# Kernel tuning notes

Hardware: AMD Instinct MI355X
Metric: run time of the kernel (lower is better)

## Reference

```python
import jax, jax.numpy as jnp
import numpy as np

HIDDEN = 512
QK_DIM = HIDDEN // 8  # 64
B, H, W = 32, 32, 32


def conv1x1(x, w, b):
    # 1x1 conv == channel matmul: w [out_c, in_c], x [b, in_c, h, w]
    return jnp.einsum('oc,bchw->bohw', w, x) + b[None, :, None, None]


def setup_inputs() -> dict:
    key = jax.random.key(0)
    ks = jax.random.split(key, 10)
    s = 0.02
    return {
        'x': jax.random.normal(ks[0], (B, HIDDEN, H, W), jnp.float32),
        'pos_embedding': jax.random.normal(ks[1], (1, HIDDEN, 32, 32), jnp.float32),
        'query_w': jax.random.normal(ks[2], (QK_DIM, HIDDEN), jnp.float32) * s,
        'query_b': jax.random.normal(ks[3], (QK_DIM,), jnp.float32) * s,
        'key_w': jax.random.normal(ks[4], (QK_DIM, HIDDEN), jnp.float32) * s,
        'key_b': jax.random.normal(ks[5], (QK_DIM,), jnp.float32) * s,
        'value_w': jax.random.normal(ks[6], (HIDDEN, HIDDEN), jnp.float32) * s,
        'value_b': jax.random.normal(ks[7], (HIDDEN,), jnp.float32) * s,
        'out_w': jax.random.normal(ks[8], (HIDDEN, HIDDEN), jnp.float32) * s,
        'out_b': jax.random.normal(ks[9], (HIDDEN,), jnp.float32) * s,
    }


def reference(x, pos_embedding, query_w, query_b, key_w, key_b,
              value_w, value_b, out_w, out_b):
    b, c, h, w = x.shape
    n = h * w
    x = x + pos_embedding[:, :, :h, :w]
    q = conv1x1(x, query_w, query_b).reshape(b, -1, n)   # [b, d, n]
    k = conv1x1(x, key_w, key_b).reshape(b, -1, n)       # [b, d, n]
    v = conv1x1(x, value_w, value_b).reshape(b, -1, n)   # [b, c, n]
    # scores[b,i,j] = sum_d q[b,d,i] * k[b,d,j]  (no 1/sqrt(d) scaling, faithful)
    scores = jnp.einsum('bdi,bdj->bij', q, k)
    attn = jax.nn.softmax(scores, axis=-1)               # [b, n, n]
    # out[b,c,i] = sum_j v[b,c,j] * attn[b,i,j]
    out = jnp.einsum('bcj,bij->bci', v, attn).reshape(b, c, h, w)
    return conv1x1(out, out_w, out_b)
```

## Files before the change

kernel.cpp:

```cpp
#include <hip/hip_runtime.h>

#define BB 32
#define CC 512
#define DD 64
#define NN 1024
#define GRP 16
#define NGRP (BB / GRP)

typedef float4 f4;
typedef __attribute__((ext_vector_type(8))) short bf16x8;
typedef __attribute__((ext_vector_type(4))) float f32x4;
typedef __attribute__((ext_vector_type(4))) unsigned short us4;
typedef __attribute__((ext_vector_type(8))) unsigned short us8;

__device__ inline unsigned short bf16rn(float f) {
  union { float f; unsigned u; } v; v.f = f;
  unsigned r = v.u + 0x7fff + ((v.u >> 16) & 1);
  return (unsigned short)(r >> 16);
}

__device__ inline void gl_lds16(const void* g, void* l) {
  __builtin_amdgcn_global_load_lds(
      (const __attribute__((address_space(1))) unsigned int*)g,
      (__attribute__((address_space(3))) unsigned int*)l, 16, 0, 0);
}

template <int KDIM>
__device__ inline void gemm_core(const unsigned short* __restrict__ A,
                                 const unsigned short* __restrict__ Bt,
                                 int m0, int n0, int tid,
                                 unsigned short* sA, unsigned short* sB,
                                 f32x4 acc[4][4]) {
  const int wave = tid >> 6, lane = tid & 63;
  const int wm = (wave & 1) * 64, wn = (wave >> 1) * 64;
  const int fm = lane & 15;
  const int kq = lane >> 4;
  const int srow = lane >> 3;
  const int sg   = (lane & 7) ^ srow;

  for (int k0 = 0; k0 < KDIM; k0 += 64) {
#pragma unroll
    for (int t = 0; t < 4; ++t) {
      const int R = wave * 32 + t * 8;
      gl_lds16(A  + (size_t)(m0 + R + srow) * KDIM + k0 + sg * 8, sA + R * 64);
      gl_lds16(Bt + (size_t)(n0 + R + srow) * KDIM + k0 + sg * 8, sB + R * 64);
    }
    __syncthreads();
#pragma unroll
    for (int ks = 0; ks < 2; ++ks) {
      bf16x8 af[4], bfr[4];
#pragma unroll
      for (int i = 0; i < 4; ++i) {
        const int ra = wm + i * 16 + fm;
        const int rb = wn + i * 16 + fm;
        af[i]  = *(const bf16x8*)(sA + ra * 64 + ((ks * 4 + kq) ^ (ra & 7)) * 8);
        bfr[i] = *(const bf16x8*)(sB + rb * 64 + ((ks * 4 + kq) ^ (rb & 7)) * 8);
      }
#pragma unroll
      for (int i = 0; i < 4; ++i)
#pragma unroll
        for (int j = 0; j < 4; ++j)
          acc[i][j] = __builtin_amdgcn_mfma_f32_16x16x32_bf16(af[i], bfr[j], acc[i][j], 0, 0, 0);
    }
    __syncthreads();
  }
}

__global__ __launch_bounds__(256) void prep_w(
    const float* __restrict__ qw, const float* __restrict__ kw, const float* __restrict__ vw,
    const float* __restrict__ qb, const float* __restrict__ kb, const float* __restrict__ vb,
    const float* __restrict__ ow,
    unsigned short* __restrict__ wcat, unsigned short* __restrict__ owb,
    float* __restrict__ bcat) {
  int idx = blockIdx.x * 256 + threadIdx.x;
  if (idx < 640 * 512) {
    int row = idx >> 9;
    float v = (row < 64) ? qw[idx] : (row < 128) ? kw[idx - 64 * 512] : vw[idx - 128 * 512];
    wcat[idx] = bf16rn(v);
    if (idx < 640) bcat[idx] = (idx < 64) ? qb[idx] : (idx < 128) ? kb[idx - 64] : vb[idx - 128];
  } else {
    int j = idx - 640 * 512;
    owb[j] = bf16rn(ow[j]);
  }
}

__global__ __launch_bounds__(256) void prep_x(const float* __restrict__ x,
                                              const float* __restrict__ pos,
                                              unsigned short* __restrict__ A) {
  __shared__ float t[64][65];
  const int b = blockIdx.z, i0 = blockIdx.x * 64, c0 = blockIdx.y * 64;
  const int tid = threadIdx.x;
  const int ci = tid >> 4, il = (tid & 15) * 4;
  const float* xb = x + (size_t)b * CC * NN;
#pragma unroll
  for (int r = 0; r < 4; ++r) {
    int cl = r * 16 + ci;
    f4 xv = *(const f4*)(xb  + (size_t)(c0 + cl) * NN + i0 + il);
    f4 pv = *(const f4*)(pos + (size_t)(c0 + cl) * NN + i0 + il);
    t[cl][il + 0] = xv.x + pv.x;
    t[cl][il + 1] = xv.y + pv.y;
    t[cl][il + 2] = xv.z + pv.z;
    t[cl][il + 3] = xv.w + pv.w;
  }
  __syncthreads();
  const int iw = tid >> 2, cw = (tid & 3) * 16;
  unsigned short* dst = A + ((size_t)b * NN + i0 + iw) * CC + c0 + cw;
  us8 p0, p1;
#pragma unroll
  for (int j = 0; j < 8; ++j) p0[j] = bf16rn(t[cw + j][iw]);
#pragma unroll
  for (int j = 0; j < 8; ++j) p1[j] = bf16rn(t[cw + 8 + j][iw]);
  *(us8*)dst = p0;
  *(us8*)(dst + 8) = p1;
}

__global__ __launch_bounds__(256) void proj_gemm(
    const unsigned short* __restrict__ A, const unsigned short* __restrict__ wcat,
    const float* __restrict__ bcat,
    unsigned short* __restrict__ qo, unsigned short* __restrict__ ko,
    unsigned short* __restrict__ vto) {
  __shared__ unsigned short sA[8192], sB[8192];
  const int b = blockIdx.z, m0 = blockIdx.x * 128, n0 = blockIdx.y * 128;
  const int tid = threadIdx.x, wave = tid >> 6, lane = tid & 63;
  f32x4 acc[4][4];
#pragma unroll
  for (int i = 0; i < 4; ++i)
#pragma unroll
    for (int j = 0; j < 4; ++j) acc[i][j] = (f32x4)(0.0f);

  gemm_core<512>(A + (size_t)b * NN * CC, wcat, m0, n0, tid, sA, sB, acc);

  const int wm = (wave & 1) * 64, wn = (wave >> 1) * 64;
#pragma unroll
  for (int i = 0; i < 4; ++i)
#pragma unroll
    for (int j = 0; j < 4; ++j) {
      int col  = n0 + wn + j * 16 + (lane & 15);
      int rowb = m0 + wm + i * 16 + (lane >> 4) * 4;
      float bias = bcat[col];
      if (col < 64) {
#pragma unroll
        for (int r = 0; r < 4; ++r)
          qo[((size_t)b * NN + rowb + r) * DD + col] = bf16rn(acc[i][j][r] + bias);
      } else if (col < 128) {
#pragma unroll
        for (int r = 0; r < 4; ++r)
          ko[((size_t)b * NN + rowb + r) * DD + col - 64] = bf16rn(acc[i][j][r] + bias);
      } else {
        int c = col - 128;
        us4 pk;
#pragma unroll
        for (int r = 0; r < 4; ++r) pk[r] = bf16rn(acc[i][j][r] + bias);
        *(us4*)(vto + ((size_t)b * CC + c) * NN + rowb) = pk;
      }
    }
}

__global__ __launch_bounds__(256) void stats_kernel(
    const unsigned short* __restrict__ q, const unsigned short* __restrict__ k,
    float2* __restrict__ stats) {
  __shared__ unsigned short sQ[128 * 64];
  __shared__ unsigned short sK[128 * 64];
  __shared__ float2 wred[4][128];

  const int b = blockIdx.y, i0 = blockIdx.x * 128;
  const int tid = threadIdx.x, wave = tid >> 6, lane = tid & 63;
  const int wm = (wave & 1) * 64, wn = (wave >> 1) * 64;
  const int fm = lane & 15, kq = lane >> 4;
  const int srow = lane >> 3, sg = (lane & 7) ^ srow;

  const unsigned short* qb = q + (size_t)b * NN * DD;
  const unsigned short* kb = k + (size_t)b * NN * DD;

#pragma unroll
  for (int t = 0; t < 4; ++t) {
    const int R = wave * 32 + t * 8;
    gl_lds16(qb + (size_t)(i0 + R + srow) * DD + sg * 8, sQ + R * 64);
  }

  bf16x8 aq[4][2];
  float m_l[4][4], l_l[4][4];
#pragma unroll
  for (int i = 0; i < 4; ++i)
#pragma unroll
    for (int r = 0; r < 4; ++r) { m_l[i][r] = -1e30f; l_l[i][r] = 0.f; }

  for (int jt = 0; jt < 8; ++jt) {
    const int j0 = jt * 128;
#pragma unroll
    for (int t = 0; t < 4; ++t) {
      const int R = wave * 32 + t * 8;
      gl_lds16(kb + (size_t)(j0 + R + srow) * DD + sg * 8, sK + R * 64);
    }
    __syncthreads();
    if (jt == 0) {
#pragma unroll
      for (int i = 0; i < 4; ++i)
#pragma unroll
        for (int kd = 0; kd < 2; ++kd) {
          const int ra = wm + i * 16 + fm;
          aq[i][kd] = *(const bf16x8*)(sQ + ra * 64 + ((kd * 4 + kq) ^ (ra & 7)) * 8);
        }
    }
    f32x4 S[4][4];
#pragma unroll
    for (int i = 0; i < 4; ++i)
#pragma unroll
      for (int j = 0; j < 4; ++j) S[i][j] = (f32x4)(0.0f);
#pragma unroll
    for (int kd = 0; kd < 2; ++kd) {
      bf16x8 bk[4];
#pragma unroll
      for (int j = 0; j < 4; ++j) {
        const int rb = wn + j * 16 + fm;
        bk[j] = *(const bf16x8*)(sK + rb * 64 + ((kd * 4 + kq) ^ (rb & 7)) * 8);
      }
#pragma unroll
      for (int i = 0; i < 4; ++i)
#pragma unroll
        for (int j = 0; j < 4; ++j)
          S[i][j] = __builtin_amdgcn_mfma_f32_16x16x32_bf16(aq[i][kd], bk[j], S[i][j], 0, 0, 0);
    }
#pragma unroll
    for (int i = 0; i < 4; ++i)
#pragma unroll
      for (int r = 0; r < 4; ++r) {
        float v0 = S[0 * 0 + i][0][r], v1 = S[i][1][r], v2 = S[i][2][r], v3 = S[i][3][r];
        float mt = fmaxf(fmaxf(v0, v1), fmaxf(v2, v3));
        float lt = __expf(v0 - mt) + __expf(v1 - mt) + __expf(v2 - mt) + __expf(v3 - mt);
        float mo = m_l[i][r];
        float mn = fmaxf(mo, mt);
        l_l[i][r] = l_l[i][r] * __expf(mo - mn) + lt * __expf(mt - mn);
        m_l[i][r] = mn;
      }
    __syncthreads();
  }

#pragma unroll
  for (int i = 0; i < 4; ++i)
#pragma unroll
    for (int r = 0; r < 4; ++r) {
      float m = m_l[i][r], l = l_l[i][r];
#pragma unroll
      for (int off = 1; off < 16; off <<= 1) {
        float mo = __shfl_xor(m, off, 64);
        float lo = __shfl_xor(l, off, 64);
        float mn = fmaxf(m, mo);
        l = l * __expf(m - mn) + lo * __expf(mo - mn);
        m = mn;
      }
      m_l[i][r] = m; l_l[i][r] = l;
    }
  if ((lane & 15) == 0) {
#pragma unroll
    for (int i = 0; i < 4; ++i)
#pragma unroll
      for (int r = 0; r < 4; ++r) {
        float2 p; p.x = m_l[i][r]; p.y = l_l[i][r];
        wred[wave][wm + i * 16 + kq * 4 + r] = p;
      }
  }
  __syncthreads();
  if (tid < 128) {
    const int a = tid >> 6;
    float2 p0 = wred[a][tid], p1 = wred[a + 2][tid];
    float mn = fmaxf(p0.x, p1.x);
    float l = p0.y * __expf(p0.x - mn) + p1.y * __expf(p1.x - mn);
    float2 o; o.x = mn; o.y = l;
    stats[(size_t)b * NN + i0 + tid] = o;
  }
}

__global__ __launch_bounds__(256) void pnorm_kernel(
    const unsigned short* __restrict__ q, const unsigned short* __restrict__ k,
    const float2* __restrict__ stats, unsigned short* __restrict__ P) {
  __shared__ unsigned short sQ[128 * 64];
  __shared__ unsigned short sK[128 * 64];

  const int b = blockIdx.y, i0 = blockIdx.x * 128;
  const int tid = threadIdx.x, wave = tid >> 6, lane = tid & 63;
  const int wm = (wave & 1) * 64, wn = (wave >> 1) * 64;
  const int fm = lane & 15, kq = lane >> 4;
  const int srow = lane >> 3, sg = (lane & 7) ^ srow;

  const unsigned short* qb = q + (size_t)b * NN * DD;
  const unsigned short* kb = k + (size_t)b * NN * DD;

#pragma unroll
  for (int t = 0; t < 4; ++t) {
    const int R = wave * 32 + t * 8;
    gl_lds16(qb + (size_t)(i0 + R + srow) * DD + sg * 8, sQ + R * 64);
  }

  float mrow[4][4], irow[4][4];
#pragma unroll
  for (int i = 0; i < 4; ++i)
#pragma unroll
    for (int r = 0; r < 4; ++r) {
      float2 st = stats[(size_t)b * NN + i0 + wm + i * 16 + kq * 4 + r];
      mrow[i][r] = st.x; irow[i][r] = 1.0f / st.y;
    }

  bf16x8 aq[4][2];
  for (int jt = 0; jt < 8; ++jt) {
    const int j0 = jt * 128;
#pragma unroll
    for (int t = 0; t < 4; ++t) {
      const int R = wave * 32 + t * 8;
      gl_lds16(kb + (size_t)(j0 + R + srow) * DD + sg * 8, sK + R * 64);
    }
    __syncthreads();
    if (jt == 0) {
#pragma unroll
      for (int i = 0; i < 4; ++i)
#pragma unroll
        for (int kd = 0; kd < 2; ++kd) {
          const int ra = wm + i * 16 + fm;
          aq[i][kd] = *(const bf16x8*)(sQ + ra * 64 + ((kd * 4 + kq) ^ (ra & 7)) * 8);
        }
    }
    f32x4 S[4][4];
#pragma unroll
    for (int i = 0; i < 4; ++i)
#pragma unroll
      for (int j = 0; j < 4; ++j) S[i][j] = (f32x4)(0.0f);
#pragma unroll
    for (int kd = 0; kd < 2; ++kd) {
      bf16x8 bk[4];
#pragma unroll
      for (int j = 0; j < 4; ++j) {
        const int rb = wn + j * 16 + fm;
        bk[j] = *(const bf16x8*)(sK + rb * 64 + ((kd * 4 + kq) ^ (rb & 7)) * 8);
      }
#pragma unroll
      for (int i = 0; i < 4; ++i)
#pragma unroll
        for (int j = 0; j < 4; ++j)
          S[i][j] = __builtin_amdgcn_mfma_f32_16x16x32_bf16(aq[i][kd], bk[j], S[i][j], 0, 0, 0);
    }
#pragma unroll
    for (int i = 0; i < 4; ++i)
#pragma unroll
      for (int j = 0; j < 4; ++j) {
        const int col = j0 + wn + j * 16 + fm;
#pragma unroll
        for (int r = 0; r < 4; ++r) {
          const int row = i0 + wm + i * 16 + kq * 4 + r;
          P[((size_t)b * NN + row) * NN + col] =
              bf16rn(__expf(S[i][j][r] - mrow[i][r]) * irow[i][r]);
        }
      }
    __syncthreads();
  }
}

__global__ __launch_bounds__(256) void pv_gemm(
    const unsigned short* __restrict__ P, const unsigned short* __restrict__ vT,
    unsigned short* __restrict__ attnout) {
  __shared__ unsigned short sA[8192], sB[8192];
  const int b = blockIdx.z, m0 = blockIdx.x * 128, n0 = blockIdx.y * 128;
  const int tid = threadIdx.x, wave = tid >> 6, lane = tid & 63;
  f32x4 acc[4][4];
#pragma unroll
  for (int i = 0; i < 4; ++i)
#pragma unroll
    for (int j = 0; j < 4; ++j) acc[i][j] = (f32x4)(0.0f);

  gemm_core<1024>(P + (size_t)b * NN * NN, vT + (size_t)b * CC * NN, m0, n0, tid, sA, sB, acc);

  const int wm = (wave & 1) * 64, wn = (wave >> 1) * 64;
#pragma unroll
  for (int i = 0; i < 4; ++i)
#pragma unroll
    for (int j = 0; j < 4; ++j) {
      int col  = n0 + wn + j * 16 + (lane & 15);
      int rowb = m0 + wm + i * 16 + (lane >> 4) * 4;
#pragma unroll
      for (int r = 0; r < 4; ++r)
        attnout[((size_t)b * NN + rowb + r) * CC + col] = bf16rn(acc[i][j][r]);
    }
}

__global__ __launch_bounds__(256) void outproj_gemm(
    const unsigned short* __restrict__ owb, const unsigned short* __restrict__ attnout,
    const float* __restrict__ ob, float* __restrict__ out) {
  __shared__ unsigned short sA[8192], sB[8192];
  const int b = blockIdx.z, m0 = blockIdx.x * 128, n0 = blockIdx.y * 128;
  const int tid = threadIdx.x, wave = tid >> 6, lane = tid & 63;
  f32x4 acc[4][4];
#pragma unroll
  for (int i = 0; i < 4; ++i)
#pragma unroll
    for (int j = 0; j < 4; ++j) acc[i][j] = (f32x4)(0.0f);

  gemm_core<512>(owb, attnout + (size_t)b * NN * CC, m0, n0, tid, sA, sB, acc);

  const int wm = (wave & 1) * 64, wn = (wave >> 1) * 64;
#pragma unroll
  for (int i = 0; i < 4; ++i)
#pragma unroll
    for (int j = 0; j < 4; ++j) {
      int col  = n0 + wn + j * 16 + (lane & 15);
      int rowb = m0 + wm + i * 16 + (lane >> 4) * 4;
      f4 b4 = *(const f4*)(ob + rowb);
#pragma unroll
      for (int r = 0; r < 4; ++r)
        out[((size_t)b * CC + rowb + r) * NN + col] = acc[i][j][r] + ((const float*)&b4)[r];
    }
}

extern "C" void kernel_launch(void* const* d_in, const int* in_sizes, int n_in,
                              void* d_out, int out_size, void* d_ws, size_t ws_size,
                              hipStream_t stream) {
  const float* x   = (const float*)d_in[0];
  const float* pos = (const float*)d_in[1];
  const float* qw  = (const float*)d_in[2];
  const float* qb  = (const float*)d_in[3];
  const float* kw  = (const float*)d_in[4];
  const float* kb  = (const float*)d_in[5];
  const float* vw  = (const float*)d_in[6];
  const float* vb  = (const float*)d_in[7];
  const float* ow  = (const float*)d_in[8];
  const float* ob  = (const float*)d_in[9];
  float* out = (float*)d_out;

  char* w = (char*)d_ws;
  unsigned short* wcat = (unsigned short*)w; w += (size_t)640 * 512 * 2;
  unsigned short* owb  = (unsigned short*)w; w += (size_t)512 * 512 * 2;
  float*          bcat = (float*)w;          w += 640 * 4;
  unsigned short* A    = (unsigned short*)w; w += (size_t)BB * NN * CC * 2;
  unsigned short* q    = (unsigned short*)w; w += (size_t)BB * NN * DD * 2;
  unsigned short* k    = (unsigned short*)w; w += (size_t)BB * NN * DD * 2;
  unsigned short* vT   = (unsigned short*)w; w += (size_t)BB * CC * NN * 2;
  float2*        stats = (float2*)w;         w += (size_t)BB * NN * 8;
  unsigned short* PG   = (unsigned short*)w; w += (size_t)GRP * NN * NN * 2;
  unsigned short* attnout = A;

  hipLaunchKernelGGL(prep_w, dim3(2304), dim3(256), 0, stream,
                     qw, kw, vw, qb, kb, vb, ow, wcat, owb, bcat);
  hipLaunchKernelGGL(prep_x, dim3(16, 8, 32), dim3(256), 0, stream, x, pos, A);
  hipLaunchKernelGGL(proj_gemm, dim3(8, 5, 32), dim3(256), 0, stream,
                     A, wcat, bcat, q, k, vT);
  hipLaunchKernelGGL(stats_kernel, dim3(8, 32), dim3(256), 0, stream, q, k, stats);

  for (int g = 0; g < NGRP; ++g) {
    const unsigned short* qg  = q  + (size_t)g * GRP * NN * DD;
    const unsigned short* kg  = k  + (size_t)g * GRP * NN * DD;
    const unsigned short* vTg = vT + (size_t)g * GRP * CC * NN;
    const float2*         stg = stats + (size_t)g * GRP * NN;
    unsigned short* aog = attnout + (size_t)g * GRP * NN * CC;
    hipLaunchKernelGGL(pnorm_kernel, dim3(8, GRP), dim3(256), 0, stream, qg, kg, stg, PG);
    hipLaunchKernelGGL(pv_gemm, dim3(8, 4, GRP), dim3(256), 0, stream, PG, vTg, aog);
  }

  hipLaunchKernelGGL(outproj_gemm, dim3(4, 8, 32), dim3(256), 0, stream,
                     owb, attnout, ob, out);
}
```

Before: 325.2 us.

## Double-buffer LDS tiles to overlap global loads with MFMA compute

Converts the shared GEMM core and the stats and pnorm kernels to a two-stage LDS ping-pong. The next K tile is issued via global_load_lds before computing on the current one, with a vmcnt wait plus barrier at the end of each step. This hides global-load latency behind MFMA work, and Q fragments are now loaded once outside the loop. In exchange LDS use per block doubles (64KB for the GEMMs), which may lower occupancy.

```diff
diff --git a/kernel.cpp b/kernel.cpp
--- a/kernel.cpp
+++ b/kernel.cpp
@@ -23,6 +23,11 @@
   __builtin_amdgcn_global_load_lds(
       (const __attribute__((address_space(1))) unsigned int*)g,
       (__attribute__((address_space(3))) unsigned int*)l, 16, 0, 0);
+}
+
+__device__ inline void wait_prefetch_and_barrier() {
+  asm volatile("s_waitcnt vmcnt(0)" ::: "memory");
+  __builtin_amdgcn_s_barrier();
 }
 
 template <int KDIM>
@@ -38,14 +43,26 @@
   const int srow = lane >> 3;
   const int sg   = (lane & 7) ^ srow;
 
-  for (int k0 = 0; k0 < KDIM; k0 += 64) {
+  const unsigned short* ga = A  + (size_t)(m0 + srow) * KDIM + sg * 8;
+  const unsigned short* gb = Bt + (size_t)(n0 + srow) * KDIM + sg * 8;
+
+  auto stage = [&](int buf, int k0) {
 #pragma unroll
     for (int t = 0; t < 4; ++t) {
       const int R = wave * 32 + t * 8;
-      gl_lds16(A  + (size_t)(m0 + R + srow) * KDIM + k0 + sg * 8, sA + R * 64);
-      gl_lds16(Bt + (size_t)(n0 + R + srow) * KDIM + k0 + sg * 8, sB + R * 64);
-    }
-    __syncthreads();
+      gl_lds16(ga + (size_t)R * KDIM + k0, sA + buf * 8192 + R * 64);
+      gl_lds16(gb + (size_t)R * KDIM + k0, sB + buf * 8192 + R * 64);
+    }
+  };
+
+  stage(0, 0);
+  wait_prefetch_and_barrier();
+
+  int cur = 0;
+  for (int k0 = 0; k0 < KDIM; k0 += 64) {
+    if (k0 + 64 < KDIM) stage(cur ^ 1, k0 + 64);
+    const unsigned short* pA = sA + cur * 8192;
+    const unsigned short* pB = sB + cur * 8192;
 #pragma unroll
     for (int ks = 0; ks < 2; ++ks) {
       bf16x8 af[4], bfr[4];
@@ -53,8 +70,8 @@
       for (int i = 0; i < 4; ++i) {
         const int ra = wm + i * 16 + fm;
         const int rb = wn + i * 16 + fm;
-        af[i]  = *(const bf16x8*)(sA + ra * 64 + ((ks * 4 + kq) ^ (ra & 7)) * 8);
-        bfr[i] = *(const bf16x8*)(sB + rb * 64 + ((ks * 4 + kq) ^ (rb & 7)) * 8);
+        af[i]  = *(const bf16x8*)(pA + ra * 64 + ((ks * 4 + kq) ^ (ra & 7)) * 8);
+        bfr[i] = *(const bf16x8*)(pB + rb * 64 + ((ks * 4 + kq) ^ (rb & 7)) * 8);
       }
 #pragma unroll
       for (int i = 0; i < 4; ++i)
@@ -62,7 +79,8 @@
         for (int j = 0; j < 4; ++j)
           acc[i][j] = __builtin_amdgcn_mfma_f32_16x16x32_bf16(af[i], bfr[j], acc[i][j], 0, 0, 0);
     }
-    __syncthreads();
+    wait_prefetch_and_barrier();
+    cur ^= 1;
   }
 }
 
@@ -119,7 +137,7 @@
     const float* __restrict__ bcat,
     unsigned short* __restrict__ qo, unsigned short* __restrict__ ko,
     unsigned short* __restrict__ vto) {
-  __shared__ unsigned short sA[8192], sB[8192];
+  __shared__ unsigned short sA[16384], sB[16384];
   const int b = blockIdx.z, m0 = blockIdx.x * 128, n0 = blockIdx.y * 128;
   const int tid = threadIdx.x, wave = tid >> 6, lane = tid & 63;
   f32x4 acc[4][4];
@@ -159,8 +177,8 @@
 __global__ __launch_bounds__(256) void stats_kernel(
     const unsigned short* __restrict__ q, const unsigned short* __restrict__ k,
     float2* __restrict__ stats) {
-  __shared__ unsigned short sQ[128 * 64];
-  __shared__ unsigned short sK[128 * 64];
+  __shared__ unsigned short sQ[8192];
+  __shared__ unsigned short sK[16384];
   __shared__ float2 wred[4][128];
 
   const int b = blockIdx.y, i0 = blockIdx.x * 128;
@@ -171,37 +189,42 @@
 
   const unsigned short* qb = q + (size_t)b * NN * DD;
   const unsigned short* kb = k + (size_t)b * NN * DD;
+
+  auto stageK = [&](int buf, int j0) {
+#pragma unroll
+    for (int t = 0; t < 4; ++t) {
+      const int R = wave * 32 + t * 8;
+      gl_lds16(kb + (size_t)(j0 + R + srow) * DD + sg * 8, sK + buf * 8192 + R * 64);
+    }
+  };
 
 #pragma unroll
   for (int t = 0; t < 4; ++t) {
     const int R = wave * 32 + t * 8;
     gl_lds16(qb + (size_t)(i0 + R + srow) * DD + sg * 8, sQ + R * 64);
   }
+  stageK(0, 0);
+  wait_prefetch_and_barrier();
 
   bf16x8 aq[4][2];
+#pragma unroll
+  for (int i = 0; i < 4; ++i)
+#pragma unroll
+    for (int kd = 0; kd < 2; ++kd) {
+      const int ra = wm + i * 16 + fm;
+      aq[i][kd] = *(const bf16x8*)(sQ + ra * 64 + ((kd * 4 + kq) ^ (ra & 7)) * 8);
+    }
+
   float m_l[4][4], l_l[4][4];
 #pragma unroll
   for (int i = 0; i < 4; ++i)
 #pragma unroll
     for (int r = 0; r < 4; ++r) { m_l[i][r] = -1e30f; l_l[i][r] = 0.f; }
 
+  int cur = 0;
   for (int jt = 0; jt < 8; ++jt) {
-    const int j0 = jt * 128;
-#pragma unroll
-    for (int t = 0; t < 4; ++t) {
-      const int R = wave * 32 + t * 8;
-      gl_lds16(kb + (size_t)(j0 + R + srow) * DD + sg * 8, sK + R * 64);
-    }
-    __syncthreads();
-    if (jt == 0) {
-#pragma unroll
-      for (int i = 0; i < 4; ++i)
-#pragma unroll
-        for (int kd = 0; kd < 2; ++kd) {
-          const int ra = wm + i * 16 + fm;
-          aq[i][kd] = *(const bf16x8*)(sQ + ra * 64 + ((kd * 4 + kq) ^ (ra & 7)) * 8);
-        }
-    }
+    if (jt < 7) stageK(cur ^ 1, (jt + 1) * 128);
+    const unsigned short* pK = sK + cur * 8192;
     f32x4 S[4][4];
 #pragma unroll
     for (int i = 0; i < 4; ++i)
@@ -213,7 +236,7 @@
 #pragma unroll
       for (int j = 0; j < 4; ++j) {
         const int rb = wn + j * 16 + fm;
-        bk[j] = *(const bf16x8*)(sK + rb * 64 + ((kd * 4 + kq) ^ (rb & 7)) * 8);
+        bk[j] = *(const bf16x8*)(pK + rb * 64 + ((kd * 4 + kq) ^ (rb & 7)) * 8);
       }
 #pragma unroll
       for (int i = 0; i < 4; ++i)
@@ -225,7 +248,7 @@
     for (int i = 0; i < 4; ++i)
 #pragma unroll
       for (int r = 0; r < 4; ++r) {
-        float v0 = S[0 * 0 + i][0][r], v1 = S[i][1][r], v2 = S[i][2][r], v3 = S[i][3][r];
+        float v0 = S[i][0][r], v1 = S[i][1][r], v2 = S[i][2][r], v3 = S[i][3][r];
         float mt = fmaxf(fmaxf(v0, v1), fmaxf(v2, v3));
         float lt = __expf(v0 - mt) + __expf(v1 - mt) + __expf(v2 - mt) + __expf(v3 - mt);
         float mo = m_l[i][r];
@@ -233,7 +256,8 @@
         l_l[i][r] = l_l[i][r] * __expf(mo - mn) + lt * __expf(mt - mn);
         m_l[i][r] = mn;
       }
-    __syncthreads();
+    wait_prefetch_and_barrier();
+    cur ^= 1;
   }
 
 #pragma unroll
@@ -274,8 +298,8 @@
 __global__ __launch_bounds__(256) void pnorm_kernel(
     const unsigned short* __restrict__ q, const unsigned short* __restrict__ k,
     const float2* __restrict__ stats, unsigned short* __restrict__ P) {
-  __shared__ unsigned short sQ[128 * 64];
-  __shared__ unsigned short sK[128 * 64];
+  __shared__ unsigned short sQ[8192];
+  __shared__ unsigned short sK[16384];
 
   const int b = blockIdx.y, i0 = blockIdx.x * 128;
   const int tid = threadIdx.x, wave = tid >> 6, lane = tid & 63;
@@ -285,12 +309,21 @@
 
   const unsigned short* qb = q + (size_t)b * NN * DD;
   const unsigned short* kb = k + (size_t)b * NN * DD;
+
+  auto stageK = [&](int buf, int j0) {
+#pragma unroll
+    for (int t = 0; t < 4; ++t) {
+      const int R = wave * 32 + t * 8;
+      gl_lds16(kb + (size_t)(j0 + R + srow) * DD + sg * 8, sK + buf * 8192 + R * 64);
+    }
+  };
 
 #pragma unroll
   for (int t = 0; t < 4; ++t) {
     const int R = wave * 32 + t * 8;
     gl_lds16(qb + (size_t)(i0 + R + srow) * DD + sg * 8, sQ + R * 64);
   }
+  stageK(0, 0);
 
   float mrow[4][4], irow[4][4];
 #pragma unroll
@@ -301,24 +334,22 @@
       mrow[i][r] = st.x; irow[i][r] = 1.0f / st.y;
     }
 
+  wait_prefetch_and_barrier();
+
   bf16x8 aq[4][2];
+#pragma unroll
+  for (int i = 0; i < 4; ++i)
+#pragma unroll
+    for (int kd = 0; kd < 2; ++kd) {
+      const int ra = wm + i * 16 + fm;
+      aq[i][kd] = *(const bf16x8*)(sQ + ra * 64 + ((kd * 4 + kq) ^ (ra & 7)) * 8);
+    }
+
+  int cur = 0;
   for (int jt = 0; jt < 8; ++jt) {
     const int j0 = jt * 128;
-#pragma unroll
-    for (int t = 0; t < 4; ++t) {
-      const int R = wave * 32 + t * 8;
-      gl_lds16(kb + (size_t)(j0 + R + srow) * DD + sg * 8, sK + R * 64);
-    }
-    __syncthreads();
-    if (jt == 0) {
-#pragma unroll
-      for (int i = 0; i < 4; ++i)
-#pragma unroll
-        for (int kd = 0; kd < 2; ++kd) {
-          const int ra = wm + i * 16 + fm;
-          aq[i][kd] = *(const bf16x8*)(sQ + ra * 64 + ((kd * 4 + kq) ^ (ra & 7)) * 8);
-        }
-    }
+    if (jt < 7) stageK(cur ^ 1, j0 + 128);
+    const unsigned short* pK = sK + cur * 8192;
     f32x4 S[4][4];
 #pragma unroll
     for (int i = 0; i < 4; ++i)
@@ -330,7 +361,7 @@
 #pragma unroll
       for (int j = 0; j < 4; ++j) {
         const int rb = wn + j * 16 + fm;
-        bk[j] = *(const bf16x8*)(sK + rb * 64 + ((kd * 4 + kq) ^ (rb & 7)) * 8);
+        bk[j] = *(const bf16x8*)(pK + rb * 64 + ((kd * 4 + kq) ^ (rb & 7)) * 8);
       }
 #pragma unroll
       for (int i = 0; i < 4; ++i)
@@ -341,23 +372,32 @@
 #pragma unroll
     for (int i = 0; i < 4; ++i)
 #pragma unroll
+      for (int j = 0; j < 4; ++j)
+#pragma unroll
+        for (int r = 0; r < 4; ++r)
+          S[i][j][r] = __expf(S[i][j][r] - mrow[i][r]) * irow[i][r];
+
+    wait_prefetch_and_barrier();
+
+#pragma unroll
+    for (int i = 0; i < 4; ++i)
+#pragma unroll
       for (int j = 0; j < 4; ++j) {
         const int col = j0 + wn + j * 16 + fm;
 #pragma unroll
         for (int r = 0; r < 4; ++r) {
           const int row = i0 + wm + i * 16 + kq * 4 + r;
-          P[((size_t)b * NN + row) * NN + col] =
-              bf16rn(__expf(S[i][j][r] - mrow[i][r]) * irow[i][r]);
+          P[((size_t)b * NN + row) * NN + col] = bf16rn(S[i][j][r]);
         }
       }
-    __syncthreads();
+    cur ^= 1;
   }
 }
 
 __global__ __launch_bounds__(256) void pv_gemm(
     const unsigned short* __restrict__ P, const unsigned short* __restrict__ vT,
     unsigned short* __restrict__ attnout) {
-  __shared__ unsigned short sA[8192], sB[8192];
+  __shared__ unsigned short sA[16384], sB[16384];
   const int b = blockIdx.z, m0 = blockIdx.x * 128, n0 = blockIdx.y * 128;
   const int tid = threadIdx.x, wave = tid >> 6, lane = tid & 63;
   f32x4 acc[4][4];
@@ -384,7 +424,7 @@
 __global__ __launch_bounds__(256) void outproj_gemm(
     const unsigned short* __restrict__ owb, const unsigned short* __restrict__ attnout,
     const float* __restrict__ ob, float* __restrict__ out) {
-  __shared__ unsigned short sA[8192], sB[8192];
+  __shared__ unsigned short sA[16384], sB[16384];
   const int b = blockIdx.z, m0 = blockIdx.x * 128, n0 = blockIdx.y * 128;
   const int tid = threadIdx.x, wave = tid >> 6, lane = tid & 63;
   f32x4 acc[4][4];
```

Result: no change. 321.5 us (-1.2%).

## Triple-buffer GEMM LDS loads and split softmax stats and pnorm over key tiles

Applied to the files above, without the earlier changes.

The shared GEMM core now uses a three-stage LDS ring with async global-to-LDS prefetch two tiles ahead and explicit vmcnt waits, replacing the load/sync/compute/sync loop. The stats kernel is split across two key halves, writing partial max/sum pairs that pnorm merges. pnorm also gets a grid dimension per key tile instead of looping over keys. These changes aim to hide memory latency and raise occupancy/parallelism, at the cost of triple the LDS per block (96KB for GEMMs), which may cut occupancy.

```diff
diff --git a/kernel.cpp b/kernel.cpp
--- a/kernel.cpp
+++ b/kernel.cpp
@@ -31,6 +31,7 @@
                                  int m0, int n0, int tid,
                                  unsigned short* sA, unsigned short* sB,
                                  f32x4 acc[4][4]) {
+  constexpr int NT = KDIM / 64;
   const int wave = tid >> 6, lane = tid & 63;
   const int wm = (wave & 1) * 64, wn = (wave >> 1) * 64;
   const int fm = lane & 15;
@@ -38,31 +39,48 @@
   const int srow = lane >> 3;
   const int sg   = (lane & 7) ^ srow;
 
-  for (int k0 = 0; k0 < KDIM; k0 += 64) {
+  const unsigned short* ga = A  + (size_t)(m0 + srow) * KDIM + sg * 8;
+  const unsigned short* gb = Bt + (size_t)(n0 + srow) * KDIM + sg * 8;
+
+  auto stage = [&](int buf, int k0) {
 #pragma unroll
     for (int t = 0; t < 4; ++t) {
       const int R = wave * 32 + t * 8;
-      gl_lds16(A  + (size_t)(m0 + R + srow) * KDIM + k0 + sg * 8, sA + R * 64);
-      gl_lds16(Bt + (size_t)(n0 + R + srow) * KDIM + k0 + sg * 8, sB + R * 64);
-    }
-    __syncthreads();
+      gl_lds16(ga + (size_t)R * KDIM + k0, sA + buf * 8192 + R * 64);
+      gl_lds16(gb + (size_t)R * KDIM + k0, sB + buf * 8192 + R * 64);
+    }
+  };
+
+  stage(0, 0);
+  stage(1, 64);
+
+#pragma unroll
+  for (int i = 0; i < NT; ++i) {
+    if (i + 1 < NT) {
+      asm volatile("s_waitcnt vmcnt(8)" ::: "memory");
+    } else {
+      asm volatile("s_waitcnt vmcnt(0)" ::: "memory");
+    }
+    __builtin_amdgcn_s_barrier();
+    if (i + 2 < NT) stage((i + 2) % 3, (i + 2) * 64);
+    const unsigned short* pA = sA + (i % 3) * 8192;
+    const unsigned short* pB = sB + (i % 3) * 8192;
 #pragma unroll
     for (int ks = 0; ks < 2; ++ks) {
       bf16x8 af[4], bfr[4];
 #pragma unroll
-      for (int i = 0; i < 4; ++i) {
-        const int ra = wm + i * 16 + fm;
-        const int rb = wn + i * 16 + fm;
-        af[i]  = *(const bf16x8*)(sA + ra * 64 + ((ks * 4 + kq) ^ (ra & 7)) * 8);
-        bfr[i] = *(const bf16x8*)(sB + rb * 64 + ((ks * 4 + kq) ^ (rb & 7)) * 8);
-      }
-#pragma unroll
-      for (int i = 0; i < 4; ++i)
+      for (int ii = 0; ii < 4; ++ii) {
+        const int ra = wm + ii * 16 + fm;
+        const int rb = wn + ii * 16 + fm;
+        af[ii]  = *(const bf16x8*)(pA + ra * 64 + ((ks * 4 + kq) ^ (ra & 7)) * 8);
+        bfr[ii] = *(const bf16x8*)(pB + rb * 64 + ((ks * 4 + kq) ^ (rb & 7)) * 8);
+      }
+#pragma unroll
+      for (int ii = 0; ii < 4; ++ii)
 #pragma unroll
         for (int j = 0; j < 4; ++j)
-          acc[i][j] = __builtin_amdgcn_mfma_f32_16x16x32_bf16(af[i], bfr[j], acc[i][j], 0, 0, 0);
-    }
-    __syncthreads();
+          acc[ii][j] = __builtin_amdgcn_mfma_f32_16x16x32_bf16(af[ii], bfr[j], acc[ii][j], 0, 0, 0);
+    }
   }
 }
 
@@ -119,7 +137,7 @@
     const float* __restrict__ bcat,
     unsigned short* __restrict__ qo, unsigned short* __restrict__ ko,
     unsigned short* __restrict__ vto) {
-  __shared__ unsigned short sA[8192], sB[8192];
+  __shared__ unsigned short sA[24576], sB[24576];
   const int b = blockIdx.z, m0 = blockIdx.x * 128, n0 = blockIdx.y * 128;
   const int tid = threadIdx.x, wave = tid >> 6, lane = tid & 63;
   f32x4 acc[4][4];
@@ -158,12 +176,13 @@
 
 __global__ __launch_bounds__(256) void stats_kernel(
     const unsigned short* __restrict__ q, const unsigned short* __restrict__ k,
-    float2* __restrict__ stats) {
-  __shared__ unsigned short sQ[128 * 64];
-  __shared__ unsigned short sK[128 * 64];
+    float2* __restrict__ stats_part) {
+  __shared__ unsigned short sQ[8192];
+  __shared__ unsigned short sK[24576];
   __shared__ float2 wred[4][128];
 
-  const int b = blockIdx.y, i0 = blockIdx.x * 128;
+  const int b = blockIdx.z, jc = blockIdx.y, i0 = blockIdx.x * 128;
+  const int jbase = jc * 512;
   const int tid = threadIdx.x, wave = tid >> 6, lane = tid & 63;
   const int wm = (wave & 1) * 64, wn = (wave >> 1) * 64;
   const int fm = lane & 15, kq = lane >> 4;
@@ -171,12 +190,22 @@
 
   const unsigned short* qb = q + (size_t)b * NN * DD;
   const unsigned short* kb = k + (size_t)b * NN * DD;
+
+  auto stageK = [&](int buf, int j0) {
+#pragma unroll
+    for (int t = 0; t < 4; ++t) {
+      const int R = wave * 32 + t * 8;
+      gl_lds16(kb + (size_t)(j0 + R + srow) * DD + sg * 8, sK + buf * 8192 + R * 64);
+    }
+  };
 
 #pragma unroll
   for (int t = 0; t < 4; ++t) {
     const int R = wave * 32 + t * 8;
     gl_lds16(qb + (size_t)(i0 + R + srow) * DD + sg * 8, sQ + R * 64);
   }
+  stageK(0, jbase);
+  stageK(1, jbase + 128);
 
   bf16x8 aq[4][2];
   float m_l[4][4], l_l[4][4];
@@ -185,14 +214,15 @@
 #pragma unroll
     for (int r = 0; r < 4; ++r) { m_l[i][r] = -1e30f; l_l[i][r] = 0.f; }
 
-  for (int jt = 0; jt < 8; ++jt) {
-    const int j0 = jt * 128;
-#pragma unroll
-    for (int t = 0; t < 4; ++t) {
-      const int R = wave * 32 + t * 8;
-      gl_lds16(kb + (size_t)(j0 + R + srow) * DD + sg * 8, sK + R * 64);
-    }
-    __syncthreads();
+#pragma unroll
+  for (int jt = 0; jt < 4; ++jt) {
+    if (jt < 3) {
+      asm volatile("s_waitcnt vmcnt(4)" ::: "memory");
+    } else {
+      asm volatile("s_waitcnt vmcnt(0)" ::: "memory");
+    }
+    __builtin_amdgcn_s_barrier();
+    if (jt + 2 < 4) stageK((jt + 2) % 3, jbase + (jt + 2) * 128);
     if (jt == 0) {
 #pragma unroll
       for (int i = 0; i < 4; ++i)
@@ -202,6 +232,7 @@
           aq[i][kd] = *(const bf16x8*)(sQ + ra * 64 + ((kd * 4 + kq) ^ (ra & 7)) * 8);
         }
     }
+    const unsigned short* pK = sK + (jt % 3) * 8192;
     f32x4 S[4][4];
 #pragma unroll
     for (int i = 0; i < 4; ++i)
@@ -213,7 +244,7 @@
 #pragma unroll
       for (int j = 0; j < 4; ++j) {
         const int rb = wn + j * 16 + fm;
-        bk[j] = *(const bf16x8*)(sK + rb * 64 + ((kd * 4 + kq) ^ (rb & 7)) * 8);
+        bk[j] = *(const bf16x8*)(pK + rb * 64 + ((kd * 4 + kq) ^ (rb & 7)) * 8);
       }
 #pragma unroll
       for (int i = 0; i < 4; ++i)
@@ -225,7 +256,7 @@
     for (int i = 0; i < 4; ++i)
 #pragma unroll
       for (int r = 0; r < 4; ++r) {
-        float v0 = S[0 * 0 + i][0][r], v1 = S[i][1][r], v2 = S[i][2][r], v3 = S[i][3][r];
+        float v0 = S[i][0][r], v1 = S[i][1][r], v2 = S[i][2][r], v3 = S[i][3][r];
         float mt = fmaxf(fmaxf(v0, v1), fmaxf(v2, v3));
         float lt = __expf(v0 - mt) + __expf(v1 - mt) + __expf(v2 - mt) + __expf(v3 - mt);
         float mo = m_l[i][r];
@@ -233,7 +264,6 @@
         l_l[i][r] = l_l[i][r] * __expf(mo - mn) + lt * __expf(mt - mn);
         m_l[i][r] = mn;
       }
-    __syncthreads();
   }
 
 #pragma unroll
@@ -267,17 +297,17 @@
     float mn = fmaxf(p0.x, p1.x);
     float l = p0.y * __expf(p0.x - mn) + p1.y * __expf(p1.x - mn);
     float2 o; o.x = mn; o.y = l;
-    stats[(size_t)b * NN + i0 + tid] = o;
+    stats_part[((size_t)b * NN + i0 + tid) * 2 + jc] = o;
   }
 }
 
 __global__ __launch_bounds__(256) void pnorm_kernel(
     const unsigned short* __restrict__ q, const unsigned short* __restrict__ k,
-    const float2* __restrict__ stats, unsigned short* __restrict__ P) {
-  __shared__ unsigned short sQ[128 * 64];
-  __shared__ unsigned short sK[128 * 64];
-
-  const int b = blockIdx.y, i0 = blockIdx.x * 128;
+    const float2* __restrict__ stats_part, unsigned short* __restrict__ P) {
+  __shared__ unsigned short sQ[8192];
+  __shared__ unsigned short sK[8192];
+
+  const int b = blockIdx.z, i0 = blockIdx.x * 128, j0 = blockIdx.y * 128;
   const int tid = threadIdx.x, wave = tid >> 6, lane = tid & 63;
   const int wm = (wave & 1) * 64, wn = (wave >> 1) * 64;
   const int fm = lane & 15, kq = lane >> 4;
@@ -290,6 +320,7 @@
   for (int t = 0; t < 4; ++t) {
     const int R = wave * 32 + t * 8;
     gl_lds16(qb + (size_t)(i0 + R + srow) * DD + sg * 8, sQ + R * 64);
+    gl_lds16(kb + (size_t)(j0 + R + srow) * DD + sg * 8, sK + R * 64);
   }
 
   float mrow[4][4], irow[4][4];
@@ -297,67 +328,61 @@
   for (int i = 0; i < 4; ++i)
 #pragma unroll
     for (int r = 0; r < 4; ++r) {
-      float2 st = stats[(size_t)b * NN + i0 + wm + i * 16 + kq * 4 + r];
-      mrow[i][r] = st.x; irow[i][r] = 1.0f / st.y;
-    }
+      const size_t row = (size_t)b * NN + i0 + wm + i * 16 + kq * 4 + r;
+      f4 st = *(const f4*)(stats_part + row * 2);
+      float m = fmaxf(st.x, st.z);
+      float l = st.y * __expf(st.x - m) + st.w * __expf(st.z - m);
+      mrow[i][r] = m; irow[i][r] = 1.0f / l;
+    }
+
+  __syncthreads();
 
   bf16x8 aq[4][2];
-  for (int jt = 0; jt < 8; ++jt) {
-    const int j0 = jt * 128;
-#pragma unroll
-    for (int t = 0; t < 4; ++t) {
-      const int R = wave * 32 + t * 8;
-      gl_lds16(kb + (size_t)(j0 + R + srow) * DD + sg * 8, sK + R * 64);
-    }
-    __syncthreads();
-    if (jt == 0) {
-#pragma unroll
-      for (int i = 0; i < 4; ++i)
-#pragma unroll
-        for (int kd = 0; kd < 2; ++kd) {
-          const int ra = wm + i * 16 + fm;
-          aq[i][kd] = *(const bf16x8*)(sQ + ra * 64 + ((kd * 4 + kq) ^ (ra & 7)) * 8);
-        }
-    }
-    f32x4 S[4][4];
+#pragma unroll
+  for (int i = 0; i < 4; ++i)
+#pragma unroll
+    for (int kd = 0; kd < 2; ++kd) {
+      const int ra = wm + i * 16 + fm;
+      aq[i][kd] = *(const bf16x8*)(sQ + ra * 64 + ((kd * 4 + kq) ^ (ra & 7)) * 8);
+    }
+
+  f32x4 S[4][4];
+#pragma unroll
+  for (int i = 0; i < 4; ++i)
+#pragma unroll
+    for (int j = 0; j < 4; ++j) S[i][j] = (f32x4)(0.0f);
+#pragma unroll
+  for (int kd = 0; kd < 2; ++kd) {
+    bf16x8 bk[4];
+#pragma unroll
+    for (int j = 0; j < 4; ++j) {
+      const int rb = wn + j * 16 + fm;
+      bk[j] = *(const bf16x8*)(sK + rb * 64 + ((kd * 4 + kq) ^ (rb & 7)) * 8);
+    }
 #pragma unroll
     for (int i = 0; i < 4; ++i)
 #pragma unroll
-      for (int j = 0; j < 4; ++j) S[i][j] = (f32x4)(0.0f);
-#pragma unroll
-    for (int kd = 0; kd < 2; ++kd) {
-      bf16x8 bk[4];
-#pragma unroll
-      for (int j = 0; j < 4; ++j) {
-        const int rb = wn + j * 16 + fm;
-        bk[j] = *(const bf16x8*)(sK + rb * 64 + ((kd * 4 + kq) ^ (rb & 7)) * 8);
-      }
-#pragma unroll
-      for (int i = 0; i < 4; ++i)
-#pragma unroll
-        for (int j = 0; j < 4; ++j)
-          S[i][j] = __builtin_amdgcn_mfma_f32_16x16x32_bf16(aq[i][kd], bk[j], S[i][j], 0, 0, 0);
-    }
-#pragma unroll
-    for (int i = 0; i < 4; ++i)
-#pragma unroll
-      for (int j = 0; j < 4; ++j) {
-        const int col = j0 + wn + j * 16 + fm;
-#pragma unroll
-        for (int r = 0; r < 4; ++r) {
-          const int row = i0 + wm + i * 16 + kq * 4 + r;
-          P[((size_t)b * NN + row) * NN + col] =
-              bf16rn(__expf(S[i][j][r] - mrow[i][r]) * irow[i][r]);
-        }
-      }
-    __syncthreads();
-  }
+      for (int j = 0; j < 4; ++j)
+        S[i][j] = __builtin_amdgcn_mfma_f32_16x16x32_bf16(aq[i][kd], bk[j], S[i][j], 0, 0, 0);
+  }
+#pragma unroll
+  for (int i = 0; i < 4; ++i)
+#pragma unroll
+    for (int j = 0; j < 4; ++j) {
+      const int col = j0 + wn + j * 16 + fm;
+#pragma unroll
+      for (int r = 0; r < 4; ++r) {
+        const int row = i0 + wm + i * 16 + kq * 4 + r;
+        P[((size_t)b * NN + row) * NN + col] =
+            bf16rn(__expf(S[i][j][r] - mrow[i][r]) * irow[i][r]);
+      }
+    }
 }
 
 __global__ __launch_bounds__(256) void pv_gemm(
     const unsigned short* __restrict__ P, const unsigned short* __restrict__ vT,
     unsigned short* __restrict__ attnout) {
-  __shared__ unsigned short sA[8192], sB[8192];
+  __shared__ unsigned short sA[24576], sB[24576];
   const int b = blockIdx.z, m0 = blockIdx.x * 128, n0 = blockIdx.y * 128;
   const int tid = threadIdx.x, wave = tid >> 6, lane = tid & 63;
   f32x4 acc[4][4];
@@ -384,7 +409,7 @@
 __global__ __launch_bounds__(256) void outproj_gemm(
     const unsigned short* __restrict__ owb, const unsigned short* __restrict__ attnout,
     const float* __restrict__ ob, float* __restrict__ out) {
-  __shared__ unsigned short sA[8192], sB[8192];
+  __shared__ unsigned short sA[24576], sB[24576];
   const int b = blockIdx.z, m0 = blockIdx.x * 128, n0 = blockIdx.y * 128;
   const int tid = threadIdx.x, wave = tid >> 6, lane = tid & 63;
   f32x4 acc[4][4];
@@ -432,7 +457,7 @@
   unsigned short* q    = (unsigned short*)w; w += (size_t)BB * NN * DD * 2;
   unsigned short* k    = (unsigned short*)w; w += (size_t)BB * NN * DD * 2;
   unsigned short* vT   = (unsigned short*)w; w += (size_t)BB * CC * NN * 2;
-  float2*        stats = (float2*)w;         w += (size_t)BB * NN * 8;
+  float2*    stats_prt = (float2*)w;         w += (size_t)BB * NN * 2 * 8;
   unsigned short* PG   = (unsigned short*)w; w += (size_t)GRP * NN * NN * 2;
   unsigned short* attnout = A;
 
@@ -441,15 +466,15 @@
   hipLaunchKernelGGL(prep_x, dim3(16, 8, 32), dim3(256), 0, stream, x, pos, A);
   hipLaunchKernelGGL(proj_gemm, dim3(8, 5, 32), dim3(256), 0, stream,
                      A, wcat, bcat, q, k, vT);
-  hipLaunchKernelGGL(stats_kernel, dim3(8, 32), dim3(256), 0, stream, q, k, stats);
+  hipLaunchKernelGGL(stats_kernel, dim3(8, 2, 32), dim3(256), 0, stream, q, k, stats_prt);
 
   for (int g = 0; g < NGRP; ++g) {
     const unsigned short* qg  = q  + (size_t)g * GRP * NN * DD;
     const unsigned short* kg  = k  + (size_t)g * GRP * NN * DD;
     const unsigned short* vTg = vT + (size_t)g * GRP * CC * NN;
-    const float2*         stg = stats + (size_t)g * GRP * NN;
+    const float2*         stg = stats_prt + (size_t)g * GRP * NN * 2;
     unsigned short* aog = attnout + (size_t)g * GRP * NN * CC;
-    hipLaunchKernelGGL(pnorm_kernel, dim3(8, GRP), dim3(256), 0, stream, qg, kg, stg, PG);
+    hipLaunchKernelGGL(pnorm_kernel, dim3(8, 8, GRP), dim3(256), 0, stream, qg, kg, stg, PG);
     hipLaunchKernelGGL(pv_gemm, dim3(8, 4, GRP), dim3(256), 0, stream, PG, vTg, aog);
   }
 
```

After: 361.8 us. 1.11x slower.
